# Kernel tuning notes

Hardware: AMD Instinct MI355X
Metric: run time of the kernel (lower is better)

Reference implementation:

```python
import jax, jax.numpy as jnp
import numpy as np

B, S, D = 8, 2048, 512
DK = 64  # attention_dim

def setup_inputs() -> dict:
    key = jax.random.key(0)
    k0, k1, k2, k3 = jax.random.split(key, 4)
    inputs = jax.random.normal(k0, (B, S, D), dtype=jnp.float32)
    # add_weight initializer='random_normal' -> stddev 0.05 in keras
    W_q = jax.random.normal(k1, (D, DK), dtype=jnp.float32) * 0.05
    W_k = jax.random.normal(k2, (D, DK), dtype=jnp.float32) * 0.05
    W_v = jax.random.normal(k3, (D, DK), dtype=jnp.float32) * 0.05
    return {"inputs": inputs, "W_q": W_q, "W_k": W_k, "W_v": W_v}

def reference(inputs, W_q, W_k, W_v):
    # QKV projections: [B,S,D] @ [D,DK] -> [B,S,DK]
    q = jnp.einsum('bsd,dk->bsk', inputs, W_q)
    k = jnp.einsum('bsd,dk->bsk', inputs, W_k)
    v = jnp.einsum('bsd,dk->bsk', inputs, W_v)
    scale = 1.0 / jnp.sqrt(jnp.asarray(DK, dtype=q.dtype))
    scores = jnp.einsum('bqk,bsk->bqs', q, k) * scale  # [B,S,S]
    weights = jax.nn.softmax(scores, axis=-1)
    attended = jnp.einsum('bqs,bsk->bqk', weights, v)  # [B,S,DK]
    return attended, weights
```

## Files before the change

kernel.cpp:

```cpp
#include <hip/hip_runtime.h>


typedef __bf16 bf16x8 __attribute__((ext_vector_type(8)));
typedef float f32x4 __attribute__((ext_vector_type(4)));

__device__ __forceinline__ short f2bf(float f) {
    unsigned u = __builtin_bit_cast(unsigned, f);
    u = (u + 0x7fffu + ((u >> 16) & 1u)) >> 16;
    return (short)u;
}
__device__ __forceinline__ float bf2f(short h) {
    unsigned u = ((unsigned)(unsigned short)h) << 16;
    return __builtin_bit_cast(float, u);
}
__device__ __forceinline__ bf16x8 ldfrag(const short* p) {
    return *reinterpret_cast<const bf16x8*>(p);
}
__device__ __forceinline__ f32x4 mfma16(bf16x8 a, bf16x8 b, f32x4 c) {
    return __builtin_amdgcn_mfma_f32_16x16x32_bf16(a, b, c, 0, 0, 0);
}
__device__ __forceinline__ bf16x8 packbf8(f32x4 a, f32x4 b) {
    union { bf16x8 v; short s[8]; } u;
    #pragma unroll
    for (int i = 0; i < 4; i++) { u.s[i] = f2bf(a[i]); u.s[4 + i] = f2bf(b[i]); }
    return u.v;
}

__global__ void wtrans_kernel(const float* __restrict__ Wq,
                              const float* __restrict__ Wk,
                              const float* __restrict__ Wv,
                              short* __restrict__ wt_hi,
                              short* __restrict__ wt_lo) {
    int idx = blockIdx.x * 256 + threadIdx.x;
    int k = idx & 511;
    int n = (idx >> 9) & 63;
    int m = idx >> 15;
    const float* W = (m == 0) ? Wq : (m == 1) ? Wk : Wv;
    float w = W[k * 64 + n];
    short hi = f2bf(w);
    wt_hi[idx] = hi;
    if (m < 2) wt_lo[idx] = f2bf(w - bf2f(hi));
}

__global__ __launch_bounds__(256) void qkv_kernel(
    const float* __restrict__ x,
    const short* __restrict__ wt_hi, const short* __restrict__ wt_lo,
    short* __restrict__ Qg, short* __restrict__ Kg, short* __restrict__ VTg) {
  __shared__ __align__(16) short Ah[32 * 40], Al[32 * 40];
  __shared__ __align__(16) short Bqh[64 * 40], Bql[64 * 40];
  __shared__ __align__(16) short Bkh[64 * 40], Bkl[64 * 40];
  __shared__ __align__(16) short Bvh[64 * 40];
  const int t = threadIdx.x;
  const int wave = t >> 6, lane = t & 63, quad = lane >> 4, l15 = lane & 15;
  const int rg = wave & 1, ntp = wave >> 1;
  const int rbase = blockIdx.x * 32;

  f32x4 accq[2] = {}, acck[2] = {}, accv[2] = {};

  for (int k0 = 0; k0 < 512; k0 += 32) {
    {
      int row = t >> 3, off = (t & 7) << 2;
      float4 v = *(const float4*)(x + (size_t)(rbase + row) * 512 + k0 + off);
      short4 h, lo;
      h.x = f2bf(v.x); lo.x = f2bf(v.x - bf2f(h.x));
      h.y = f2bf(v.y); lo.y = f2bf(v.y - bf2f(h.y));
      h.z = f2bf(v.z); lo.z = f2bf(v.z - bf2f(h.z));
      h.w = f2bf(v.w); lo.w = f2bf(v.w - bf2f(h.w));
      *(short4*)(Ah + row * 40 + off) = h;
      *(short4*)(Al + row * 40 + off) = lo;
    }
    {
      int row = t >> 2, off = (t & 3) << 3;
      int src = row * 512 + k0 + off;
      int dst = row * 40 + off;
      *(int4*)(Bqh + dst) = *(const int4*)(wt_hi + 0 * 32768 + src);
      *(int4*)(Bkh + dst) = *(const int4*)(wt_hi + 1 * 32768 + src);
      *(int4*)(Bvh + dst) = *(const int4*)(wt_hi + 2 * 32768 + src);
      *(int4*)(Bql + dst) = *(const int4*)(wt_lo + 0 * 32768 + src);
      *(int4*)(Bkl + dst) = *(const int4*)(wt_lo + 1 * 32768 + src);
    }
    __syncthreads();
    bf16x8 ah = ldfrag(Ah + (rg * 16 + l15) * 40 + quad * 8);
    bf16x8 al = ldfrag(Al + (rg * 16 + l15) * 40 + quad * 8);
    #pragma unroll
    for (int j = 0; j < 2; j++) {
      const int nt = ntp * 2 + j;
      const int boff = (nt * 16 + l15) * 40 + quad * 8;
      bf16x8 bh = ldfrag(Bqh + boff);
      accq[j] = mfma16(ah, bh, accq[j]);
      accq[j] = mfma16(al, bh, accq[j]);
      accq[j] = mfma16(ah, ldfrag(Bql + boff), accq[j]);
      bh = ldfrag(Bkh + boff);
      acck[j] = mfma16(ah, bh, acck[j]);
      acck[j] = mfma16(al, bh, acck[j]);
      acck[j] = mfma16(ah, ldfrag(Bkl + boff), acck[j]);
      accv[j] = mfma16(ah, ldfrag(Bvh + boff), accv[j]);
    }
    __syncthreads();
  }
  #pragma unroll
  for (int j = 0; j < 2; j++) {
    const int nt = ntp * 2 + j;
    #pragma unroll
    for (int r = 0; r < 4; r++) {
      int row = rbase + rg * 16 + quad * 4 + r;
      int col = nt * 16 + l15;
      Qg[(size_t)row * 64 + col] = f2bf(accq[j][r]);
      Kg[(size_t)row * 64 + col] = f2bf(acck[j][r]);
    }
  }
  short* vt = Ah;
  #pragma unroll
  for (int j = 0; j < 2; j++) {
    const int col = (ntp * 2 + j) * 16 + l15;
    short4 p;
    p.x = f2bf(accv[j][0]); p.y = f2bf(accv[j][1]);
    p.z = f2bf(accv[j][2]); p.w = f2bf(accv[j][3]);
    *(short4*)(vt + col * 40 + rg * 16 + quad * 4) = p;
  }
  __syncthreads();
  {
    const int bidx = rbase >> 11;
    int c = t >> 2, ch = (t & 3) << 3;
    *(int4*)(VTg + (size_t)bidx * 131072 + (size_t)c * 2048 + (rbase & 2047) + ch) =
        *(const int4*)(vt + c * 40 + ch);
  }
}

__global__ __launch_bounds__(256) void attn_kernel(
    const short* __restrict__ Qg, const short* __restrict__ Kg,
    const short* __restrict__ VTg,
    float* __restrict__ att_out, float* __restrict__ w_out) {
  __shared__ __align__(16) short Qs[32 * 72];
  __shared__ __align__(16) short Ks[128 * 72];
  __shared__ __align__(16) short Vs[64 * 136];
  __shared__ __align__(16) float Pf[4][16 * 68];
  __shared__ float Lb[4][16];
  const int t = threadIdx.x;
  const int wave = t >> 6, lane = t & 63, quad = lane >> 4, l15 = lane & 15;
  const int rg = wave & 1, half = wave >> 1;
  const int b = blockIdx.x;
  const int qbase = blockIdx.y * 32;
  const float sc2 = 0.125f * 1.44269504088896340736f;
  const float C0 = 16.0f;

  {
    int row = t >> 3, off = (t & 7) << 3;
    *(int4*)(Qs + row * 72 + off) =
        *(const int4*)(Qg + (size_t)(b * 2048 + qbase + row) * 64 + off);
  }
  __syncthreads();
  const bf16x8 aq0 = ldfrag(Qs + (rg * 16 + l15) * 72 + quad * 8);
  const bf16x8 aq1 = ldfrag(Qs + (rg * 16 + l15) * 72 + 32 + quad * 8);

  float l[4] = {0.f, 0.f, 0.f, 0.f};

  for (int s0 = 0; s0 < 2048; s0 += 128) {
    #pragma unroll
    for (int i = 0; i < 4; i++) {
      int c = t + i * 256;
      int row = c >> 3, off = (c & 7) << 3;
      *(int4*)(Ks + row * 72 + off) =
          *(const int4*)(Kg + (size_t)(b * 2048 + s0 + row) * 64 + off);
    }
    __syncthreads();
    float ls[4] = {0.f, 0.f, 0.f, 0.f};
    #pragma unroll
    for (int nt2 = 0; nt2 < 4; nt2++) {
      const int nt = half * 4 + nt2;
      const int koff = (nt * 16 + l15) * 72 + quad * 8;
      f32x4 c = {};
      c = mfma16(aq0, ldfrag(Ks + koff), c);
      c = mfma16(aq1, ldfrag(Ks + koff + 32), c);
      #pragma unroll
      for (int r = 0; r < 4; r++) ls[r] += exp2f(c[r] * sc2 - C0);
    }
    #pragma unroll
    for (int r = 0; r < 4; r++) {
      float ps = ls[r];
      ps += __shfl_xor(ps, 1);
      ps += __shfl_xor(ps, 2);
      ps += __shfl_xor(ps, 4);
      ps += __shfl_xor(ps, 8);
      l[r] += ps;
    }
    __syncthreads();
  }
  if (l15 == 0) {
    #pragma unroll
    for (int r = 0; r < 4; r++) Lb[wave][quad * 4 + r] = l[r];
  }
  __syncthreads();
  float invl[4];
  #pragma unroll
  for (int r = 0; r < 4; r++)
    invl[r] = 1.0f / (Lb[wave][quad * 4 + r] + Lb[wave ^ 2][quad * 4 + r]);

  f32x4 acc[4] = {};
  float* wbase = w_out + ((size_t)b * 2048 + qbase + rg * 16) * 2048;

  for (int s0 = 0; s0 < 2048; s0 += 128) {
    #pragma unroll
    for (int i = 0; i < 4; i++) {
      int c = t + i * 256;
      int row = c >> 3, off = (c & 7) << 3;
      *(int4*)(Ks + row * 72 + off) =
          *(const int4*)(Kg + (size_t)(b * 2048 + s0 + row) * 64 + off);
    }
    #pragma unroll
    for (int i = 0; i < 4; i++) {
      int c = t + i * 256;
      int row = c >> 4, off = (c & 15) << 3;
      *(int4*)(Vs + row * 136 + off) =
          *(const int4*)(VTg + (size_t)b * 131072 + (size_t)row * 2048 + s0 + off);
    }
    __syncthreads();
    float* pf = Pf[wave];
    #pragma unroll
    for (int nt2 = 0; nt2 < 4; nt2++) {
      const int nt = half * 4 + nt2;
      const int koff = (nt * 16 + l15) * 72 + quad * 8;
      f32x4 c = {};
      c = mfma16(aq0, ldfrag(Ks + koff), c);
      c = mfma16(aq1, ldfrag(Ks + koff + 32), c);
      #pragma unroll
      for (int r = 0; r < 4; r++)
        pf[(quad * 4 + r) * 68 + nt2 * 16 + l15] =
            exp2f(c[r] * sc2 - C0) * invl[r];
    }
    #pragma unroll
    for (int i = 0; i < 4; i++) {
      int row = i * 4 + quad;
      f32x4 v = *(const f32x4*)(pf + row * 68 + l15 * 4);
      *(f32x4*)(wbase + (size_t)row * 2048 + s0 + half * 64 + l15 * 4) = v;
    }
    #pragma unroll
    for (int ks2 = 0; ks2 < 2; ks2++) {
      f32x4 p0 = *(const f32x4*)(pf + l15 * 68 + ks2 * 32 + quad * 8);
      f32x4 p1 = *(const f32x4*)(pf + l15 * 68 + ks2 * 32 + quad * 8 + 4);
      bf16x8 ap = packbf8(p0, p1);
      const int soff = half * 64 + ks2 * 32 + quad * 8;
      #pragma unroll
      for (int nc = 0; nc < 4; nc++)
        acc[nc] = mfma16(ap, ldfrag(Vs + (nc * 16 + l15) * 136 + soff), acc[nc]);
    }
    __syncthreads();
  }
  float* Ob = (float*)Pf;
  if (half == 1) {
    #pragma unroll
    for (int nc = 0; nc < 4; nc++)
      #pragma unroll
      for (int r = 0; r < 4; r++)
        Ob[(rg * 16 + quad * 4 + r) * 68 + nc * 16 + l15] = acc[nc][r];
  }
  __syncthreads();
  if (half == 0) {
    #pragma unroll
    for (int nc = 0; nc < 4; nc++)
      #pragma unroll
      for (int r = 0; r < 4; r++) {
        int row = rg * 16 + quad * 4 + r;
        att_out[((size_t)b * 2048 + qbase + row) * 64 + nc * 16 + l15] =
            acc[nc][r] + Ob[row * 68 + nc * 16 + l15];
      }
  }
}

extern "C" void kernel_launch(void* const* d_in, const int* in_sizes, int n_in,
                              void* d_out, int out_size, void* d_ws, size_t ws_size,
                              hipStream_t stream) {
  const float* x  = (const float*)d_in[0];
  const float* Wq = (const float*)d_in[1];
  const float* Wk = (const float*)d_in[2];
  const float* Wv = (const float*)d_in[3];

  char* ws = (char*)d_ws;
  short* wt_hi = (short*)(ws + 0);
  short* wt_lo = (short*)(ws + 196608);
  short* Qg    = (short*)(ws + 327680);
  short* Kg    = (short*)(ws + 327680 + 2097152);
  short* VTg   = (short*)(ws + 327680 + 4194304);

  float* att  = (float*)d_out;
  float* wout = att + (size_t)8 * 2048 * 64;

  hipLaunchKernelGGL(wtrans_kernel, dim3(384), dim3(256), 0, stream,
                     Wq, Wk, Wv, wt_hi, wt_lo);
  hipLaunchKernelGGL(qkv_kernel, dim3(512), dim3(256), 0, stream,
                     x, wt_hi, wt_lo, Qg, Kg, VTg);
  hipLaunchKernelGGL(attn_kernel, dim3(8, 64), dim3(256), 0, stream,
                     Qg, Kg, VTg, att, wout);
}
```

Measured before the change: 221.7 us.

## Load K/V fragments directly to registers, drop shared tiles and block barriers

Removes the shared-memory staging of Q, K and V tiles. Each wave now loads its MFMA fragments straight from global memory into registers and software-prefetches the next K tile while the current one is computed. It also swaps MFMA operand order so each lane holds one query row, which lets the sum-of-exponentials reduction and weight stores work without cross-lane shuffles or an fp32 LDS bounce. P now goes to a small per-wave bf16 LDS buffer, so the main loops need no block-wide barriers. The cost is more register pressure and redundant global loads across waves, served by cache instead of shared memory.

```diff
diff --git a/kernel.cpp b/kernel.cpp
--- a/kernel.cpp
+++ b/kernel.cpp
@@ -18,12 +18,6 @@
 }
 __device__ __forceinline__ f32x4 mfma16(bf16x8 a, bf16x8 b, f32x4 c) {
     return __builtin_amdgcn_mfma_f32_16x16x32_bf16(a, b, c, 0, 0, 0);
-}
-__device__ __forceinline__ bf16x8 packbf8(f32x4 a, f32x4 b) {
-    union { bf16x8 v; short s[8]; } u;
-    #pragma unroll
-    for (int i = 0; i < 4; i++) { u.s[i] = f2bf(a[i]); u.s[4 + i] = f2bf(b[i]); }
-    return u.v;
 }
 
 __global__ void wtrans_kernel(const float* __restrict__ Wq,
@@ -127,15 +121,37 @@
   }
 }
 
+__device__ __forceinline__ void loadK8(bf16x8 (&kf)[8], const short* Kb,
+                                       int s0, int half, int l15, int quad) {
+  #pragma unroll
+  for (int nt2 = 0; nt2 < 4; nt2++) {
+    const short* kp =
+        Kb + (size_t)(s0 + (half * 4 + nt2) * 16 + l15) * 64 + quad * 8;
+    kf[nt2 * 2] = ldfrag(kp);
+    kf[nt2 * 2 + 1] = ldfrag(kp + 32);
+  }
+}
+
+__device__ __forceinline__ void qkexp8(const bf16x8 (&kf)[8], bf16x8 aq0,
+                                       bf16x8 aq1, float sc2, float C0,
+                                       float (&l)[4]) {
+  #pragma unroll
+  for (int nt2 = 0; nt2 < 4; nt2++) {
+    f32x4 c = {};
+    c = mfma16(kf[nt2 * 2], aq0, c);
+    c = mfma16(kf[nt2 * 2 + 1], aq1, c);
+    #pragma unroll
+    for (int r = 0; r < 4; r++) l[r] += exp2f(c[r] * sc2 - C0);
+  }
+}
+
 __global__ __launch_bounds__(256) void attn_kernel(
     const short* __restrict__ Qg, const short* __restrict__ Kg,
     const short* __restrict__ VTg,
     float* __restrict__ att_out, float* __restrict__ w_out) {
-  __shared__ __align__(16) short Qs[32 * 72];
-  __shared__ __align__(16) short Ks[128 * 72];
-  __shared__ __align__(16) short Vs[64 * 136];
-  __shared__ __align__(16) float Pf[4][16 * 68];
+  __shared__ __align__(16) short Plds[4 * 2 * 16 * 72];
   __shared__ float Lb[4][16];
+  __shared__ float Ob[32 * 68];
   const int t = threadIdx.x;
   const int wave = t >> 6, lane = t & 63, quad = lane >> 4, l15 = lane & 15;
   const int rg = wave & 1, half = wave >> 1;
@@ -144,109 +160,75 @@
   const float sc2 = 0.125f * 1.44269504088896340736f;
   const float C0 = 16.0f;
 
+  const short* Kb = Kg + (size_t)b * 2048 * 64;
+  const short* Vb = VTg + (size_t)b * 131072;
+  const short* qp =
+      Qg + (size_t)(b * 2048 + qbase + rg * 16 + l15) * 64 + quad * 8;
+  const bf16x8 aq0 = ldfrag(qp);
+  const bf16x8 aq1 = ldfrag(qp + 32);
+
+  float l[4] = {0.f, 0.f, 0.f, 0.f};
   {
-    int row = t >> 3, off = (t & 7) << 3;
-    *(int4*)(Qs + row * 72 + off) =
-        *(const int4*)(Qg + (size_t)(b * 2048 + qbase + row) * 64 + off);
-  }
+    bf16x8 kfA[8], kfB[8];
+    loadK8(kfA, Kb, 0, half, l15, quad);
+    for (int s0 = 0; s0 < 2048; s0 += 256) {
+      loadK8(kfB, Kb, s0 + 128, half, l15, quad);
+      qkexp8(kfA, aq0, aq1, sc2, C0, l);
+      loadK8(kfA, Kb, (s0 + 256) & 2047, half, l15, quad);
+      qkexp8(kfB, aq0, aq1, sc2, C0, l);
+    }
+  }
+  float ls = (l[0] + l[1]) + (l[2] + l[3]);
+  ls += __shfl_xor(ls, 16);
+  ls += __shfl_xor(ls, 32);
+  if (lane < 16) Lb[wave][lane] = ls;
   __syncthreads();
-  const bf16x8 aq0 = ldfrag(Qs + (rg * 16 + l15) * 72 + quad * 8);
-  const bf16x8 aq1 = ldfrag(Qs + (rg * 16 + l15) * 72 + 32 + quad * 8);
-
-  float l[4] = {0.f, 0.f, 0.f, 0.f};
-
+  const float invl = 1.0f / (Lb[wave][l15] + Lb[wave ^ 2][l15]);
+
+  f32x4 acc[4] = {};
+  float* wrow =
+      w_out + ((size_t)(b * 2048 + qbase + rg * 16 + l15)) * 2048 + half * 64;
+  short* plw = Plds + wave * 2 * (16 * 72) + l15 * 72;
+  bf16x8 kf[8];
+  loadK8(kf, Kb, 0, half, l15, quad);
   for (int s0 = 0; s0 < 2048; s0 += 128) {
-    #pragma unroll
-    for (int i = 0; i < 4; i++) {
-      int c = t + i * 256;
-      int row = c >> 3, off = (c & 7) << 3;
-      *(int4*)(Ks + row * 72 + off) =
-          *(const int4*)(Kg + (size_t)(b * 2048 + s0 + row) * 64 + off);
-    }
-    __syncthreads();
-    float ls[4] = {0.f, 0.f, 0.f, 0.f};
+    short* pl = plw + ((s0 >> 7) & 1) * (16 * 72);
+    bf16x8 vf[8];
+    #pragma unroll
+    for (int ks2 = 0; ks2 < 2; ks2++)
+      #pragma unroll
+      for (int nc = 0; nc < 4; nc++)
+        vf[ks2 * 4 + nc] = ldfrag(Vb + (size_t)(nc * 16 + l15) * 2048 + s0 +
+                                  half * 64 + ks2 * 32 + quad * 8);
+    f32x4 cc[4];
     #pragma unroll
     for (int nt2 = 0; nt2 < 4; nt2++) {
-      const int nt = half * 4 + nt2;
-      const int koff = (nt * 16 + l15) * 72 + quad * 8;
       f32x4 c = {};
-      c = mfma16(aq0, ldfrag(Ks + koff), c);
-      c = mfma16(aq1, ldfrag(Ks + koff + 32), c);
-      #pragma unroll
-      for (int r = 0; r < 4; r++) ls[r] += exp2f(c[r] * sc2 - C0);
-    }
-    #pragma unroll
-    for (int r = 0; r < 4; r++) {
-      float ps = ls[r];
-      ps += __shfl_xor(ps, 1);
-      ps += __shfl_xor(ps, 2);
-      ps += __shfl_xor(ps, 4);
-      ps += __shfl_xor(ps, 8);
-      l[r] += ps;
-    }
-    __syncthreads();
-  }
-  if (l15 == 0) {
-    #pragma unroll
-    for (int r = 0; r < 4; r++) Lb[wave][quad * 4 + r] = l[r];
-  }
-  __syncthreads();
-  float invl[4];
-  #pragma unroll
-  for (int r = 0; r < 4; r++)
-    invl[r] = 1.0f / (Lb[wave][quad * 4 + r] + Lb[wave ^ 2][quad * 4 + r]);
-
-  f32x4 acc[4] = {};
-  float* wbase = w_out + ((size_t)b * 2048 + qbase + rg * 16) * 2048;
-
-  for (int s0 = 0; s0 < 2048; s0 += 128) {
-    #pragma unroll
-    for (int i = 0; i < 4; i++) {
-      int c = t + i * 256;
-      int row = c >> 3, off = (c & 7) << 3;
-      *(int4*)(Ks + row * 72 + off) =
-          *(const int4*)(Kg + (size_t)(b * 2048 + s0 + row) * 64 + off);
-    }
-    #pragma unroll
-    for (int i = 0; i < 4; i++) {
-      int c = t + i * 256;
-      int row = c >> 4, off = (c & 15) << 3;
-      *(int4*)(Vs + row * 136 + off) =
-          *(const int4*)(VTg + (size_t)b * 131072 + (size_t)row * 2048 + s0 + off);
-    }
-    __syncthreads();
-    float* pf = Pf[wave];
+      c = mfma16(kf[nt2 * 2], aq0, c);
+      c = mfma16(kf[nt2 * 2 + 1], aq1, c);
+      cc[nt2] = c;
+    }
+    loadK8(kf, Kb, (s0 + 128) & 2047, half, l15, quad);
     #pragma unroll
     for (int nt2 = 0; nt2 < 4; nt2++) {
-      const int nt = half * 4 + nt2;
-      const int koff = (nt * 16 + l15) * 72 + quad * 8;
-      f32x4 c = {};
-      c = mfma16(aq0, ldfrag(Ks + koff), c);
-      c = mfma16(aq1, ldfrag(Ks + koff + 32), c);
-      #pragma unroll
-      for (int r = 0; r < 4; r++)
-        pf[(quad * 4 + r) * 68 + nt2 * 16 + l15] =
-            exp2f(c[r] * sc2 - C0) * invl[r];
-    }
-    #pragma unroll
-    for (int i = 0; i < 4; i++) {
-      int row = i * 4 + quad;
-      f32x4 v = *(const f32x4*)(pf + row * 68 + l15 * 4);
-      *(f32x4*)(wbase + (size_t)row * 2048 + s0 + half * 64 + l15 * 4) = v;
-    }
+      f32x4 w;
+      #pragma unroll
+      for (int r = 0; r < 4; r++) w[r] = exp2f(cc[nt2][r] * sc2 - C0) * invl;
+      *(f32x4*)(wrow + s0 + nt2 * 16 + quad * 4) = w;
+      short4 pb;
+      pb.x = f2bf(w[0]); pb.y = f2bf(w[1]);
+      pb.z = f2bf(w[2]); pb.w = f2bf(w[3]);
+      *(short4*)(pl + nt2 * 16 + quad * 4) = pb;
+    }
+    asm volatile("s_waitcnt lgkmcnt(0)" ::: "memory");
     #pragma unroll
     for (int ks2 = 0; ks2 < 2; ks2++) {
-      f32x4 p0 = *(const f32x4*)(pf + l15 * 68 + ks2 * 32 + quad * 8);
-      f32x4 p1 = *(const f32x4*)(pf + l15 * 68 + ks2 * 32 + quad * 8 + 4);
-      bf16x8 ap = packbf8(p0, p1);
-      const int soff = half * 64 + ks2 * 32 + quad * 8;
+      bf16x8 ap = ldfrag(pl + ks2 * 32 + quad * 8);
       #pragma unroll
       for (int nc = 0; nc < 4; nc++)
-        acc[nc] = mfma16(ap, ldfrag(Vs + (nc * 16 + l15) * 136 + soff), acc[nc]);
-    }
-    __syncthreads();
-  }
-  float* Ob = (float*)Pf;
+        acc[nc] = mfma16(ap, vf[ks2 * 4 + nc], acc[nc]);
+    }
+  }
   if (half == 1) {
     #pragma unroll
     for (int nc = 0; nc < 4; nc++)
@@ -261,7 +243,7 @@
       #pragma unroll
       for (int r = 0; r < 4; r++) {
         int row = rg * 16 + quad * 4 + r;
-        att_out[((size_t)b * 2048 + qbase + row) * 64 + nc * 16 + l15] =
+        att_out[((size_t)(b * 2048 + qbase + row)) * 64 + nc * 16 + l15] =
             acc[nc][r] + Ob[row * 68 + nc * 16 + l15];
       }
   }
```

After: 267.0 us. 20.4% more time.
